# Performance work log

Measured on AMD Instinct MI355X. Metric: run time of the kernel, lower is better.

## Reference

```python
import jax, jax.numpy as jnp
import numpy as np

NUM_SPLITS = 64
UNITS_PER_SPLIT = 64
IN_DIM = 4096          # divisible by NUM_SPLITS -> 64 input features per split
OUT_DIM = NUM_SPLITS * UNITS_PER_SPLIT  # 4096
BATCH = 4096
BN_EPS = 1e-3          # keras BatchNormalization default epsilon


def make_mask():
    # block_diag of NUM_SPLITS ones-blocks of shape (IN_DIM//NUM_SPLITS, UNITS_PER_SPLIT)
    din_per = IN_DIM // NUM_SPLITS
    return jnp.kron(jnp.eye(NUM_SPLITS, dtype=jnp.float32),
                    jnp.ones((din_per, UNITS_PER_SPLIT), dtype=jnp.float32))


def setup_inputs() -> dict:
    key = jax.random.key(0)
    k_x, k_w = jax.random.split(key)
    x = jax.random.normal(k_x, (BATCH, IN_DIM), dtype=jnp.float32)
    weight = jax.random.normal(k_w, (IN_DIM, OUT_DIM), dtype=jnp.float32) * (2.0 / IN_DIM) ** 0.5
    bias = jnp.full((OUT_DIM,), 0.1, dtype=jnp.float32)
    gamma = jnp.ones((OUT_DIM,), dtype=jnp.float32)
    beta = jnp.zeros((OUT_DIM,), dtype=jnp.float32)
    return {"x": x, "weight": weight, "bias": bias, "gamma": gamma, "beta": beta}


def reference(x, weight, bias, gamma, beta):
    mask = make_mask()  # [IN_DIM, OUT_DIM] block-diagonal 0/1
    # masked dense: only block-diagonal entries of weight participate
    out = jnp.matmul(x, weight * mask) + bias  # [B, OUT_DIM]
    # BatchNorm, training=True: batch statistics (biased variance), keras eps=1e-3
    mean = jnp.mean(out, axis=0)
    var = jnp.mean(jnp.square(out - mean), axis=0)
    out = (out - mean) * jax.lax.rsqrt(var + BN_EPS) * gamma + beta
    return jax.nn.relu(out)
```

## Files before the change

kernel.cpp:

```cpp
#include <hip/hip_runtime.h>

#define BATCH 4096
#define DIM 4096
#define NSPLIT 64
#define ROWS_PB 128
#define NCHUNK 32
#define BN_EPS 1e-3f

typedef __attribute__((ext_vector_type(8))) short bf16x8;
typedef __attribute__((ext_vector_type(4))) float f32x4;

__device__ inline unsigned short f2bf(float f) {
    union { float f; unsigned int u; } c; c.f = f;
    unsigned int u = c.u;
    u += 0x7FFFu + ((u >> 16) & 1u);
    return (unsigned short)(u >> 16);
}

__global__ __launch_bounds__(256) void gemm_stats(
    const float* __restrict__ x, const float* __restrict__ w,
    float* __restrict__ part, float* __restrict__ out)
{
    __shared__ unsigned short xs[ROWS_PB][72];
    __shared__ unsigned short wt[64][72];
    __shared__ float red1[4][64], red2[4][64];

    const int s  = blockIdx.y;
    const int r0 = blockIdx.x * ROWS_PB;
    const int t  = threadIdx.x;
    const int lane = t & 63, wave = t >> 6;
    const int quad = lane >> 4, l16 = lane & 15;

    for (int i = t; i < 1024; i += 256) {
        int k = i >> 4, c4 = i & 15;
        float4 v = *(const float4*)(w + (size_t)(s*64 + k) * DIM + s*64 + c4*4);
        wt[c4*4 + 0][k] = f2bf(v.x);
        wt[c4*4 + 1][k] = f2bf(v.y);
        wt[c4*4 + 2][k] = f2bf(v.z);
        wt[c4*4 + 3][k] = f2bf(v.w);
    }

    #pragma unroll
    for (int it = 0; it < 8; it++) {
        int i = t + it * 256;
        int row = i >> 4, c4 = i & 15;
        float4 v = *(const float4*)(x + (size_t)(r0 + row) * DIM + s*64 + c4*4);
        ushort4 u;
        u.x = f2bf(v.x); u.y = f2bf(v.y); u.z = f2bf(v.z); u.w = f2bf(v.w);
        *(ushort4*)&xs[row][c4*4] = u;
    }
    __syncthreads();

    f32x4 acc[2][4];
    #pragma unroll
    for (int rt = 0; rt < 2; rt++)
        #pragma unroll
        for (int ct = 0; ct < 4; ct++)
            acc[rt][ct] = (f32x4){0.f, 0.f, 0.f, 0.f};

    bf16x8 af[2][2], bfr[4][2];
    #pragma unroll
    for (int rt = 0; rt < 2; rt++)
        #pragma unroll
        for (int kk = 0; kk < 2; kk++)
            af[rt][kk] = *(const bf16x8*)&xs[wave*32 + rt*16 + l16][kk*32 + quad*8];
    #pragma unroll
    for (int ct = 0; ct < 4; ct++)
        #pragma unroll
        for (int kk = 0; kk < 2; kk++)
            bfr[ct][kk] = *(const bf16x8*)&wt[ct*16 + l16][kk*32 + quad*8];

    #pragma unroll
    for (int kk = 0; kk < 2; kk++)
        #pragma unroll
        for (int rt = 0; rt < 2; rt++)
            #pragma unroll
            for (int ct = 0; ct < 4; ct++)
                acc[rt][ct] = __builtin_amdgcn_mfma_f32_16x16x32_bf16(
                    af[rt][kk], bfr[ct][kk], acc[rt][ct], 0, 0, 0);

    #pragma unroll
    for (int rt = 0; rt < 2; rt++)
        #pragma unroll
        for (int ct = 0; ct < 4; ct++) {
            int col = ct*16 + l16;
            #pragma unroll
            for (int r = 0; r < 4; r++) {
                int row = r0 + wave*32 + rt*16 + quad*4 + r;
                out[(size_t)row * DIM + s*64 + col] = acc[rt][ct][r];
            }
        }

    float s1[4], s2[4];
    #pragma unroll
    for (int ct = 0; ct < 4; ct++) { s1[ct] = 0.f; s2[ct] = 0.f; }
    #pragma unroll
    for (int rt = 0; rt < 2; rt++)
        #pragma unroll
        for (int ct = 0; ct < 4; ct++)
            #pragma unroll
            for (int r = 0; r < 4; r++) {
                float v = acc[rt][ct][r];
                s1[ct] += v; s2[ct] += v * v;
            }
    #pragma unroll
    for (int ct = 0; ct < 4; ct++) {
        float a = s1[ct], b = s2[ct];
        a += __shfl_xor(a, 16); b += __shfl_xor(b, 16);
        a += __shfl_xor(a, 32); b += __shfl_xor(b, 32);
        if (quad == 0) {
            red1[wave][ct*16 + l16] = a;
            red2[wave][ct*16 + l16] = b;
        }
    }
    __syncthreads();
    if (t < 64) {
        float a = red1[0][t] + red1[1][t] + red1[2][t] + red1[3][t];
        float b = red2[0][t] + red2[1][t] + red2[2][t] + red2[3][t];
        size_t base = (size_t)(s * NCHUNK + blockIdx.x) * 128;
        part[base + t]      = a;
        part[base + 64 + t] = b;
    }
}

__global__ __launch_bounds__(256) void bn_apply(
    const float* __restrict__ part, const float* __restrict__ gamma,
    const float* __restrict__ beta, float* __restrict__ out)
{
    __shared__ float scol[64], shcol[64];

    const int s  = blockIdx.y;
    const int r0 = blockIdx.x * ROWS_PB;
    const int t  = threadIdx.x;

    if (t < 64) {
        float a = 0.f, b = 0.f;
        #pragma unroll 8
        for (int p = 0; p < NCHUNK; p++) {
            size_t base = (size_t)(s * NCHUNK + p) * 128;
            a += part[base + t];
            b += part[base + 64 + t];
        }
        float mean = a * (1.f / BATCH);
        float var  = b * (1.f / BATCH) - mean * mean;
        float rstd = rsqrtf(var + BN_EPS);
        float sc = gamma[s*64 + t] * rstd;
        scol[t]  = sc;
        shcol[t] = beta[s*64 + t] - mean * sc;
    }
    __syncthreads();

    #pragma unroll
    for (int it = 0; it < 8; it++) {
        int i = t + it * 256;
        int row = i >> 4, c4 = i & 15;
        float* p = out + (size_t)(r0 + row) * DIM + s*64 + c4*4;
        float4 v = *(const float4*)p;
        int c0 = c4*4;
        v.x = fmaxf(fmaf(v.x, scol[c0+0], shcol[c0+0]), 0.f);
        v.y = fmaxf(fmaf(v.y, scol[c0+1], shcol[c0+1]), 0.f);
        v.z = fmaxf(fmaf(v.z, scol[c0+2], shcol[c0+2]), 0.f);
        v.w = fmaxf(fmaf(v.w, scol[c0+3], shcol[c0+3]), 0.f);
        *(float4*)p = v;
    }
}

extern "C" void kernel_launch(void* const* d_in, const int* in_sizes, int n_in,
                              void* d_out, int out_size, void* d_ws, size_t ws_size,
                              hipStream_t stream) {
    const float* x     = (const float*)d_in[0];
    const float* w     = (const float*)d_in[1];
    const float* gamma = (const float*)d_in[3];
    const float* beta  = (const float*)d_in[4];
    float* out  = (float*)d_out;
    float* part = (float*)d_ws;

    gemm_stats<<<dim3(NCHUNK, NSPLIT), 256, 0, stream>>>(x, w, part, out);
    bn_apply<<<dim3(NCHUNK, NSPLIT), 256, 0, stream>>>(part, gamma, beta, out);
}
```

Measured before the change: 185.2 us.

## Store GEMM intermediate as packed bf16 and load x straight into MFMA registers

```diff
diff --git a/kernel.cpp b/kernel.cpp
--- a/kernel.cpp
+++ b/kernel.cpp
@@ -8,6 +8,7 @@
 #define BN_EPS 1e-3f
 
 typedef __attribute__((ext_vector_type(8))) short bf16x8;
+typedef __attribute__((ext_vector_type(8))) unsigned short ushort8;
 typedef __attribute__((ext_vector_type(4))) float f32x4;
 
 __device__ inline unsigned short f2bf(float f) {
@@ -17,11 +18,16 @@
     return (unsigned short)(u >> 16);
 }
 
+__device__ inline float bf2f(unsigned short h) {
+    union { unsigned int u; float f; } c;
+    c.u = (unsigned int)h << 16;
+    return c.f;
+}
+
 __global__ __launch_bounds__(256) void gemm_stats(
     const float* __restrict__ x, const float* __restrict__ w,
     float* __restrict__ part, float* __restrict__ out)
 {
-    __shared__ unsigned short xs[ROWS_PB][72];
     __shared__ unsigned short wt[64][72];
     __shared__ float red1[4][64], red2[4][64];
 
@@ -40,16 +46,40 @@
         wt[c4*4 + 3][k] = f2bf(v.w);
     }
 
-    #pragma unroll
-    for (int it = 0; it < 8; it++) {
-        int i = t + it * 256;
-        int row = i >> 4, c4 = i & 15;
-        float4 v = *(const float4*)(x + (size_t)(r0 + row) * DIM + s*64 + c4*4);
-        ushort4 u;
-        u.x = f2bf(v.x); u.y = f2bf(v.y); u.z = f2bf(v.z); u.w = f2bf(v.w);
-        *(ushort4*)&xs[row][c4*4] = u;
-    }
-    __syncthreads();
+    float4 xv[2][2][2];
+    #pragma unroll
+    for (int rt = 0; rt < 2; rt++)
+        #pragma unroll
+        for (int kk = 0; kk < 2; kk++)
+            #pragma unroll
+            for (int h = 0; h < 2; h++)
+                xv[rt][kk][h] = *(const float4*)(
+                    x + (size_t)(r0 + wave*32 + rt*16 + l16) * DIM
+                      + s*64 + kk*32 + quad*8 + h*4);
+
+    __syncthreads();
+
+    bf16x8 af[2][2], bfr[4][2];
+    #pragma unroll
+    for (int rt = 0; rt < 2; rt++)
+        #pragma unroll
+        for (int kk = 0; kk < 2; kk++) {
+            bf16x8 a;
+            a[0] = (short)f2bf(xv[rt][kk][0].x);
+            a[1] = (short)f2bf(xv[rt][kk][0].y);
+            a[2] = (short)f2bf(xv[rt][kk][0].z);
+            a[3] = (short)f2bf(xv[rt][kk][0].w);
+            a[4] = (short)f2bf(xv[rt][kk][1].x);
+            a[5] = (short)f2bf(xv[rt][kk][1].y);
+            a[6] = (short)f2bf(xv[rt][kk][1].z);
+            a[7] = (short)f2bf(xv[rt][kk][1].w);
+            af[rt][kk] = a;
+        }
+    #pragma unroll
+    for (int ct = 0; ct < 4; ct++)
+        #pragma unroll
+        for (int kk = 0; kk < 2; kk++)
+            bfr[ct][kk] = *(const bf16x8*)&wt[ct*16 + l16][kk*32 + quad*8];
 
     f32x4 acc[2][4];
     #pragma unroll
@@ -57,18 +87,6 @@
         #pragma unroll
         for (int ct = 0; ct < 4; ct++)
             acc[rt][ct] = (f32x4){0.f, 0.f, 0.f, 0.f};
-
-    bf16x8 af[2][2], bfr[4][2];
-    #pragma unroll
-    for (int rt = 0; rt < 2; rt++)
-        #pragma unroll
-        for (int kk = 0; kk < 2; kk++)
-            af[rt][kk] = *(const bf16x8*)&xs[wave*32 + rt*16 + l16][kk*32 + quad*8];
-    #pragma unroll
-    for (int ct = 0; ct < 4; ct++)
-        #pragma unroll
-        for (int kk = 0; kk < 2; kk++)
-            bfr[ct][kk] = *(const bf16x8*)&wt[ct*16 + l16][kk*32 + quad*8];
 
     #pragma unroll
     for (int kk = 0; kk < 2; kk++)
@@ -80,16 +98,21 @@
                     af[rt][kk], bfr[ct][kk], acc[rt][ct], 0, 0, 0);
 
     #pragma unroll
-    for (int rt = 0; rt < 2; rt++)
-        #pragma unroll
-        for (int ct = 0; ct < 4; ct++) {
-            int col = ct*16 + l16;
-            #pragma unroll
-            for (int r = 0; r < 4; r++) {
-                int row = r0 + wave*32 + rt*16 + quad*4 + r;
-                out[(size_t)row * DIM + s*64 + col] = acc[rt][ct][r];
-            }
-        }
+    for (int j = 0; j < 4; j++) {
+        const int f0 = 2*j, f1 = 2*j + 1;
+        const f32x4 a0 = acc[f0 >> 2][f0 & 3];
+        const f32x4 a1 = acc[f1 >> 2][f1 & 3];
+        ushort8 pk;
+        pk[0] = f2bf(a0[0]); pk[1] = f2bf(a0[1]);
+        pk[2] = f2bf(a0[2]); pk[3] = f2bf(a0[3]);
+        pk[4] = f2bf(a1[0]); pk[5] = f2bf(a1[1]);
+        pk[6] = f2bf(a1[2]); pk[7] = f2bf(a1[3]);
+        int u = j*256 + t;
+        unsigned short* dst =
+            (unsigned short*)(out + (size_t)(r0 + (u >> 4)) * DIM + s*64)
+            + (u & 15) * 8;
+        *(ushort8*)dst = pk;
+    }
 
     float s1[4], s2[4];
     #pragma unroll
@@ -127,20 +150,44 @@
     const float* __restrict__ part, const float* __restrict__ gamma,
     const float* __restrict__ beta, float* __restrict__ out)
 {
+    __shared__ float redA[4][64], redB[4][64];
     __shared__ float scol[64], shcol[64];
 
     const int s  = blockIdx.y;
     const int r0 = blockIdx.x * ROWS_PB;
     const int t  = threadIdx.x;
+    const int lane = t & 63, wave = t >> 6;
+    const int quad = lane >> 4, l16 = lane & 15;
+
+    ushort8 yv[4];
+    #pragma unroll
+    for (int j = 0; j < 4; j++) {
+        int u = j*256 + t;
+        const unsigned short* src =
+            (const unsigned short*)(out + (size_t)(r0 + (u >> 4)) * DIM + s*64)
+            + (u & 15) * 8;
+        yv[j] = *(const ushort8*)src;
+    }
+
+    {
+        float a = 0.f, b = 0.f;
+        #pragma unroll
+        for (int p8 = 0; p8 < 8; p8++) {
+            int p = wave*8 + p8;
+            size_t base = (size_t)(s * NCHUNK + p) * 128;
+            a += part[base + lane];
+            b += part[base + 64 + lane];
+        }
+        redA[wave][lane] = a;
+        redB[wave][lane] = b;
+    }
+
+    asm volatile("s_waitcnt vmcnt(0)" ::: "memory");
+    __syncthreads();
 
     if (t < 64) {
-        float a = 0.f, b = 0.f;
-        #pragma unroll 8
-        for (int p = 0; p < NCHUNK; p++) {
-            size_t base = (size_t)(s * NCHUNK + p) * 128;
-            a += part[base + t];
-            b += part[base + 64 + t];
-        }
+        float a = redA[0][t] + redA[1][t] + redA[2][t] + redA[3][t];
+        float b = redB[0][t] + redB[1][t] + redB[2][t] + redB[3][t];
         float mean = a * (1.f / BATCH);
         float var  = b * (1.f / BATCH) - mean * mean;
         float rstd = rsqrtf(var + BN_EPS);
@@ -151,17 +198,20 @@
     __syncthreads();
 
     #pragma unroll
-    for (int it = 0; it < 8; it++) {
-        int i = t + it * 256;
-        int row = i >> 4, c4 = i & 15;
-        float* p = out + (size_t)(r0 + row) * DIM + s*64 + c4*4;
-        float4 v = *(const float4*)p;
-        int c0 = c4*4;
-        v.x = fmaxf(fmaf(v.x, scol[c0+0], shcol[c0+0]), 0.f);
-        v.y = fmaxf(fmaf(v.y, scol[c0+1], shcol[c0+1]), 0.f);
-        v.z = fmaxf(fmaf(v.z, scol[c0+2], shcol[c0+2]), 0.f);
-        v.w = fmaxf(fmaf(v.w, scol[c0+3], shcol[c0+3]), 0.f);
-        *(float4*)p = v;
+    for (int j = 0; j < 4; j++) {
+        #pragma unroll
+        for (int h = 0; h < 2; h++) {
+            const int f  = 2*j + h;
+            const int rt = f >> 2, ct = f & 3;
+            const int col = ct*16 + l16;
+            const float sc = scol[col], sh = shcol[col];
+            #pragma unroll
+            for (int r = 0; r < 4; r++) {
+                float v = fmaxf(fmaf(bf2f((unsigned short)yv[j][h*4 + r]), sc, sh), 0.f);
+                int row = r0 + wave*32 + rt*16 + quad*4 + r;
+                out[(size_t)row * DIM + s*64 + col] = v;
+            }
+        }
     }
 }
 
```

After: 177.5 us, median of 2. 4.2% less time.
